# Optimization experiments

Measured on AMD Instinct MI355X. Metric: run time of the kernel, lower is better.

The kernel has to match this reference:

```python
import jax, jax.numpy as jnp
import numpy as np

D_MODEL = 1024
D_STATE = 128
D_CONV = 4
EXPAND = 2
HEADDIM = 64
D_INNER = EXPAND * D_MODEL          # 2048
NHEADS = D_INNER // HEADDIM          # 32
CONV_CH = D_INNER + 2 * D_STATE      # conv acts on x, B, C (ngroups=1)
D_IN_PROJ = 2 * D_INNER + 2 * D_STATE + NHEADS
CHUNK = 128


def setup_inputs() -> dict:
    key = jax.random.key(0)
    ks = jax.random.split(key, 8)
    B, L = 4, 2048
    return {
        'x': jax.random.normal(ks[0], (B, L, D_MODEL), jnp.float32),
        'ln_w': jnp.ones((D_MODEL,), jnp.float32),
        'ln_b': jnp.zeros((D_MODEL,), jnp.float32),
        'in_proj_w': jax.random.normal(ks[1], (D_IN_PROJ, D_MODEL), jnp.float32) * 0.02,
        'conv_w': jax.random.normal(ks[2], (CONV_CH, D_CONV), jnp.float32) * 0.2,
        'conv_b': jnp.zeros((CONV_CH,), jnp.float32),
        'dt_bias': jax.random.normal(ks[3], (NHEADS,), jnp.float32) * 0.5,
        'A_log': jax.random.uniform(ks[4], (NHEADS,), jnp.float32, 0.0, 1.5),
        'D': jax.random.normal(ks[5], (NHEADS,), jnp.float32) * 0.1 + 1.0,
        'norm_w': jnp.ones((D_INNER,), jnp.float32),
        'out_proj_w': jax.random.normal(ks[6], (D_MODEL, D_INNER), jnp.float32) * 0.02,
    }


def segsum(a):
    # a: (..., T) -> (..., T, T) with out[i, j] = sum_{j < k <= i} a[k], -inf above diag
    T = a.shape[-1]
    a_rep = jnp.broadcast_to(a[..., :, None], a.shape + (T,))
    a_masked = jnp.where(jnp.tril(jnp.ones((T, T), bool), -1), a_rep, 0.0)
    seg = jnp.cumsum(a_masked, axis=-2)
    return jnp.where(jnp.tril(jnp.ones((T, T), bool), 0), seg, -jnp.inf)


def _ssd(X, a, Bm, Cm):
    # Chunked SSD (Mamba2). X: (b,l,h,p) pre-multiplied by dt; a: (b,l,h)=dt*A; Bm,Cm: (b,l,n)
    b, l, h, p = X.shape
    c = l // CHUNK
    Xc = X.reshape(b, c, CHUNK, h, p)
    Bc = Bm.reshape(b, c, CHUNK, -1)
    Cc = Cm.reshape(b, c, CHUNK, -1)
    ac = a.reshape(b, c, CHUNK, h).transpose(0, 3, 1, 2)   # (b,h,c,q)
    a_cs = jnp.cumsum(ac, axis=-1)                          # (b,h,c,q)
    Lm = jnp.exp(segsum(ac))                                # (b,h,c,q,q)
    # intra-chunk (diagonal) part
    Y_diag = jnp.einsum('bcln,bcsn,bhcls,bcshp->bclhp', Cc, Bc, Lm, Xc)
    # chunk final states
    decay_states = jnp.exp(a_cs[..., -1:] - a_cs)           # (b,h,c,q)
    states = jnp.einsum('bcln,bhcl,bclhp->bchpn', Bc, decay_states, Xc)
    states = jnp.concatenate([jnp.zeros_like(states[:, :1]), states], axis=1)  # (b,c+1,h,p,n)
    a_chunk = jnp.pad(a_cs[..., -1], ((0, 0), (0, 0), (1, 0)))  # (b,h,c+1)
    decay_chunk = jnp.exp(segsum(a_chunk))                  # (b,h,c+1,c+1)
    prev_states = jnp.einsum('bhzc,bchpn->bzhpn', decay_chunk, states)[:, :-1]  # (b,c,h,p,n)
    # inter-chunk (off-diagonal) part
    Y_off = jnp.einsum('bcln,bchpn,bhcl->bclhp', Cc, prev_states, jnp.exp(a_cs))
    return (Y_diag + Y_off).reshape(b, l, h, p)


def reference(x, ln_w, ln_b, in_proj_w, conv_w, conv_b, dt_bias, A_log, D, norm_w, out_proj_w):
    B, L, _ = x.shape
    # pre-LayerNorm
    mu = x.mean(-1, keepdims=True)
    var = ((x - mu) ** 2).mean(-1, keepdims=True)
    h = (x - mu) / jnp.sqrt(var + 1e-5) * ln_w + ln_b
    # Mamba2 in_proj -> [z, xBC, dt]
    zxbcdt = h @ in_proj_w.T
    z = zxbcdt[..., :D_INNER]
    xBC = zxbcdt[..., D_INNER:D_INNER + CONV_CH]
    dt = jax.nn.softplus(zxbcdt[..., -NHEADS:] + dt_bias)  # (B,L,H)
    # causal depthwise conv1d + SiLU
    xp = jnp.pad(xBC, ((0, 0), (D_CONV - 1, 0), (0, 0)))
    conv = sum(xp[:, k:k + L, :] * conv_w[:, k] for k in range(D_CONV)) + conv_b
    xBC = jax.nn.silu(conv)
    xs = xBC[..., :D_INNER].reshape(B, L, NHEADS, HEADDIM)
    Bm = xBC[..., D_INNER:D_INNER + D_STATE]
    Cm = xBC[..., D_INNER + D_STATE:]
    A = -jnp.exp(A_log)                                    # (H,)
    Y = _ssd(xs * dt[..., None], dt * A, Bm, Cm)
    Y = Y + D[None, None, :, None] * xs                    # D skip connection
    y = Y.reshape(B, L, D_INNER)
    # gated RMSNorm (norm_before_gate=False)
    y = y * jax.nn.silu(z)
    y = y * jax.lax.rsqrt(jnp.mean(y * y, -1, keepdims=True) + 1e-5) * norm_w
    out = y @ out_proj_w.T
    # dropout in eval mode = identity; residual
    return out + x
```

## Files before the change

kernel.cpp:

```cpp
#include <hip/hip_runtime.h>
#include <math.h>

#define BATCH   4
#define LSEQ    2048
#define DMODEL  1024
#define DSTATE  128
#define HEADDIM 64
#define DINNER  2048
#define NHEADS  32
#define CONVCH  2304
#define DINPROJ 4384
#define NPAD    4480
#define CHUNKL  128
#define NCHUNK  16
#define ROWS    (BATCH*LSEQ)

#define B_Z     ((size_t)0)
#define B_XBC   (B_Z   + (size_t)ROWS*DINNER*2)
#define B_DT    (B_XBC + (size_t)ROWS*CONVCH*2)
#define B_XS    (B_DT  + (size_t)ROWS*NHEADS*4)
#define B_BC    (B_XS  + (size_t)ROWS*DINNER*2)
#define B_Y     (B_BC  + (size_t)ROWS*256*2)
#define B_ASUM  (B_Y   + (size_t)ROWS*DINNER*2)
#define B_END   (B_ASUM + (size_t)BATCH*NCHUNK*NHEADS*4)

typedef __attribute__((ext_vector_type(8))) short bf16x8;
typedef __attribute__((ext_vector_type(4))) float f32x4;

__device__ __forceinline__ float b2f(ushort u) {
  union { uint32_t i; float f; } v; v.i = ((uint32_t)u) << 16; return v.f;
}
__device__ __forceinline__ ushort f2b(float f) {
  union { float f; uint32_t i; } v; v.f = f;
  uint32_t r = (v.i + 0x7FFFu + ((v.i >> 16) & 1u)) >> 16;
  return (ushort)r;
}

__device__ __forceinline__ void async_ld16(const void* g, void* l) {
  __builtin_amdgcn_global_load_lds(
      (const __attribute__((address_space(1))) unsigned int*)g,
      (__attribute__((address_space(3))) unsigned int*)l, 16, 0, 0);
}

template<int K>
__device__ __forceinline__ void gemm_core_swz(const ushort* __restrict__ A,
    const ushort* __restrict__ W, int m0, int n0, int tid,
    ushort* lA, ushort* lB, f32x4 acc[4][4])
{
  const int lane = tid & 63;
  const int w = tid >> 6;
  const int wm = (w & 1) * 64;
  const int wn = (w >> 1) * 64;
  const int rl = lane & 15;
  const int q  = lane >> 4;
  for (int k0 = 0; k0 < K; k0 += 64) {
    __syncthreads();
    #pragma unroll
    for (int is = 0; is < 4; is++) {
      int s = (w*4 + is)*64 + lane;
      int row = s >> 3;
      int g = (s & 7) ^ (row & 7);
      async_ld16(A + (size_t)(m0 + row)*K + k0 + g*8, lA + (size_t)s*8);
      async_ld16(W + (size_t)(n0 + row)*K + k0 + g*8, lB + (size_t)s*8);
    }
    __syncthreads();
    #pragma unroll
    for (int kh = 0; kh < 2; kh++) {
      bf16x8 af[4], bfr[4];
      #pragma unroll
      for (int i = 0; i < 4; i++) {
        int row = wm + i*16 + rl;
        af[i] = *(const bf16x8*)&lA[(size_t)(row*8 + ((kh*4 + q) ^ (row & 7)))*8];
      }
      #pragma unroll
      for (int j = 0; j < 4; j++) {
        int row = wn + j*16 + rl;
        bfr[j] = *(const bf16x8*)&lB[(size_t)(row*8 + ((kh*4 + q) ^ (row & 7)))*8];
      }
      #pragma unroll
      for (int i = 0; i < 4; i++)
        #pragma unroll
        for (int j = 0; j < 4; j++)
          acc[i][j] = __builtin_amdgcn_mfma_f32_16x16x32_bf16(af[i], bfr[j], acc[i][j], 0, 0, 0);
    }
  }
}

__global__ __launch_bounds__(256) void convert_win_kernel(const float* __restrict__ W,
                                                          ushort* __restrict__ Wb)
{
  size_t i = (size_t)blockIdx.x*256 + threadIdx.x;
  Wb[i] = (i < (size_t)DINPROJ*DMODEL) ? f2b(W[i]) : (ushort)0;
}

__global__ __launch_bounds__(256) void convert_wout_kernel(const float* __restrict__ W,
                                                           ushort* __restrict__ Wb)
{
  size_t i = (size_t)blockIdx.x*256 + threadIdx.x;
  Wb[i] = f2b(W[i]);
}

__global__ __launch_bounds__(256) void ln_kernel(const float* __restrict__ x,
    const float* __restrict__ w, const float* __restrict__ bias, ushort* __restrict__ h)
{
  const int row = blockIdx.x;
  const int t = threadIdx.x;
  const float* xr = x + (size_t)row * DMODEL;
  float v[4];
  float s = 0.f;
  #pragma unroll
  for (int i = 0; i < 4; i++) { v[i] = xr[t + i*256]; s += v[i]; }
  __shared__ float red[4];
  #pragma unroll
  for (int o = 32; o > 0; o >>= 1) s += __shfl_down(s, o, 64);
  if ((t & 63) == 0) red[t >> 6] = s;
  __syncthreads();
  float mean = (red[0]+red[1]+red[2]+red[3]) * (1.f/DMODEL);
  float vs = 0.f;
  #pragma unroll
  for (int i = 0; i < 4; i++) { float d = v[i]-mean; vs += d*d; }
  #pragma unroll
  for (int o = 32; o > 0; o >>= 1) vs += __shfl_down(vs, o, 64);
  __syncthreads();
  if ((t & 63) == 0) red[t >> 6] = vs;
  __syncthreads();
  float rstd = rsqrtf((red[0]+red[1]+red[2]+red[3]) * (1.f/DMODEL) + 1e-5f);
  ushort* hr = h + (size_t)row * DMODEL;
  #pragma unroll
  for (int i = 0; i < 4; i++) {
    int c = t + i*256;
    hr[c] = f2b((v[i]-mean)*rstd*w[c] + bias[c]);
  }
}

__global__ __launch_bounds__(256) void gemm_inproj_mfma(const ushort* __restrict__ A,
    const ushort* __restrict__ W, ushort* __restrict__ z, ushort* __restrict__ xbc,
    float* __restrict__ dtr, const float* __restrict__ dtb)
{
  __shared__ ushort smem[16384];
  ushort* lA = smem;
  ushort* lB = smem + 8192;
  const int tid = threadIdx.x;
  const int lane = tid & 63;
  const int w = tid >> 6;
  const int m0 = blockIdx.x * 128;
  const int n0 = blockIdx.y * 128;
  const int wm = (w & 1) * 64;
  const int wn = (w >> 1) * 64;
  f32x4 acc[4][4];
  #pragma unroll
  for (int i = 0; i < 4; i++)
    #pragma unroll
    for (int j = 0; j < 4; j++) acc[i][j] = (f32x4)(0.f);

  gemm_core_swz<DMODEL>(A, W, m0, n0, tid, lA, lB, acc);

  const int col_l = lane & 15;
  const int row_l = (lane >> 4) * 4;
  __syncthreads();
  if (n0 < DINNER + CONVCH) {
    #pragma unroll
    for (int i = 0; i < 4; i++)
      #pragma unroll
      for (int j = 0; j < 4; j++) {
        int col = wn + j*16 + col_l;
        int g = col >> 3;
        #pragma unroll
        for (int r = 0; r < 4; r++) {
          int row = wm + i*16 + row_l + r;
          smem[row*128 + ((g ^ (row & 7)) << 3) + (col & 7)] = f2b(acc[i][j][r]);
        }
      }
    __syncthreads();
    ushort* outp; int coff, ncols;
    if (n0 < DINNER) { outp = z;   coff = n0;          ncols = DINNER; }
    else             { outp = xbc; coff = n0 - DINNER; ncols = CONVCH; }
    #pragma unroll
    for (int it = 0; it < 8; it++) {
      int idx = tid + it*256;
      int row = idx >> 4, c8 = idx & 15;
      *(uint4*)(outp + (size_t)(m0 + row)*ncols + coff + c8*8) =
          *(const uint4*)&smem[row*128 + ((c8 ^ (row & 7)) << 3)];
    }
  } else {
    #pragma unroll
    for (int i = 0; i < 4; i++)
      #pragma unroll
      for (int j = 0; j < 2; j++) {
        int lc = wn + j*16 + col_l;
        if (lc < 32) {
          float bb = dtb[lc];
          #pragma unroll
          for (int r = 0; r < 4; r++) {
            float v = acc[i][j][r] + bb;
            v = (v > 20.f) ? v : log1pf(expf(v));
            dtr[(size_t)(m0 + wm + i*16 + row_l + r)*NHEADS + lc] = v;
          }
        }
      }
  }
}

__global__ __launch_bounds__(256) void gemm_outproj_mfma(const ushort* __restrict__ A,
    const ushort* __restrict__ W, const float* __restrict__ x, float* __restrict__ out)
{
  __shared__ ushort smem[16384];
  ushort* lA = smem;
  ushort* lB = smem + 8192;
  float* fbuf = (float*)smem;
  const int tid = threadIdx.x;
  const int lane = tid & 63;
  const int w = tid >> 6;
  const int m0 = blockIdx.x * 128;
  const int n0 = blockIdx.y * 128;
  const int wn = (w >> 1) * 64;
  f32x4 acc[4][4];
  #pragma unroll
  for (int i = 0; i < 4; i++)
    #pragma unroll
    for (int j = 0; j < 4; j++) acc[i][j] = (f32x4)(0.f);

  gemm_core_swz<DINNER>(A, W, m0, n0, tid, lA, lB, acc);

  const int colL = lane & 15;
  const int rowQ = (lane >> 4) * 4;
  #pragma unroll
  for (int h0 = 0; h0 < 2; h0++) {
    __syncthreads();
    if ((w & 1) == h0) {
      #pragma unroll
      for (int i = 0; i < 4; i++)
        #pragma unroll
        for (int j = 0; j < 4; j++) {
          int col = wn + j*16 + colL;
          int g = col >> 2;
          #pragma unroll
          for (int r = 0; r < 4; r++) {
            int row = i*16 + rowQ + r;
            fbuf[row*128 + ((g ^ (row & 7)) << 2) + (col & 3)] = acc[i][j][r];
          }
        }
    }
    __syncthreads();
    #pragma unroll
    for (int it = 0; it < 8; it++) {
      int idx = tid + it*256;
      int row = idx >> 5, c4 = idx & 31;
      int gm = m0 + h0*64 + row;
      float4 xv = *(const float4*)(x + (size_t)gm*DMODEL + n0 + c4*4);
      float4 vv = *(const float4*)&fbuf[row*128 + ((c4 ^ (row & 7)) << 2)];
      vv.x += xv.x; vv.y += xv.y; vv.z += xv.z; vv.w += xv.w;
      *(float4*)(out + (size_t)gm*DMODEL + n0 + c4*4) = vv;
    }
  }
}

__global__ __launch_bounds__(256) void conv_tiled(const ushort* __restrict__ xbc,
    const float* __restrict__ cw, const float* __restrict__ cb,
    ushort* __restrict__ xs, ushort* __restrict__ bcb)
{
  __shared__ ushort tile[35*256];
  const int tid = threadIdx.x;
  const int ch0 = blockIdx.x * 256;
  const int row0 = blockIdx.y * 32;
  const int l0 = row0 & (LSEQ-1);
  for (int idx = tid; idx < 35*32; idx += 256) {
    int r = idx >> 5, c16 = idx & 31;
    uint4 v = make_uint4(0,0,0,0);
    if (l0 + r - 3 >= 0)
      v = *(const uint4*)(xbc + (size_t)(row0 + r - 3)*CONVCH + ch0 + c16*8);
    *(uint4*)&tile[r*256 + c16*8] = v;
  }
  __syncthreads();
  const int ch = ch0 + tid;
  const float w0 = cw[ch*4+0], w1 = cw[ch*4+1], w2 = cw[ch*4+2], w3 = cw[ch*4+3];
  const float bias = cb[ch];
  const bool isX = (ch0 < DINNER);
  #pragma unroll 4
  for (int r = 0; r < 32; r++) {
    float acc = bias;
    acc = fmaf(b2f(tile[(r+0)*256 + tid]), w0, acc);
    acc = fmaf(b2f(tile[(r+1)*256 + tid]), w1, acc);
    acc = fmaf(b2f(tile[(r+2)*256 + tid]), w2, acc);
    acc = fmaf(b2f(tile[(r+3)*256 + tid]), w3, acc);
    float v = acc / (1.f + expf(-acc));
    if (isX) xs[(size_t)(row0 + r)*DINNER + ch] = f2b(v);
    else     bcb[(size_t)(row0 + r)*256 + (ch - DINNER)] = f2b(v);
  }
}

__global__ __launch_bounds__(256) void states_mfma(
    const ushort* __restrict__ xs, const ushort* __restrict__ bcb, const float* __restrict__ dt,
    const float* __restrict__ A_log, ushort* __restrict__ S, float* __restrict__ asum)
{
  constexpr int LDP = 136;
  __shared__ ushort lBT[128*LDP];
  __shared__ ushort lXT[64*LDP];
  __shared__ float dts[CHUNKL], acs[CHUNKL];
  __shared__ float wtot;
  const int hh = blockIdx.x, c = blockIdx.y, b = blockIdx.z;
  const int tid = threadIdx.x;
  const int lane = tid & 63;
  const int w = tid >> 6;
  const int rbase = b*LSEQ + c*CHUNKL;
  const size_t sbase = (size_t)((b*NCHUNK + c)*NHEADS + hh) * 8192;

  float pre = 0.f;
  if (tid < 128) {
    float myv = dt[(size_t)(rbase + tid)*NHEADS + hh];
    dts[tid] = myv;
    pre = myv;
    #pragma unroll
    for (int o = 1; o < 64; o <<= 1) {
      float u = __shfl_up(pre, o, 64);
      if ((tid & 63) >= o) pre += u;
    }
    if (tid == 63) wtot = pre;
  }
  #pragma unroll
  for (int it = 0; it < 8; it++) {
    int chunk = tid + it*256;
    int l = chunk >> 4, n8 = chunk & 15;
    ushort tmp[8];
    *(uint4*)tmp = *(const uint4*)(bcb + (size_t)(rbase + l)*256 + n8*8);
    #pragma unroll
    for (int u = 0; u < 8; u++) lBT[(n8*8+u)*LDP + l] = tmp[u];
  }
  __syncthreads();
  float alast_loc = 0.f;
  if (tid < 128) {
    float Aval = -expf(A_log[hh]);
    float a = (pre + ((tid >= 64) ? wtot : 0.f)) * Aval;
    acs[tid] = a;
    if (tid == 127) { asum[(b*NCHUNK + c)*NHEADS + hh] = a; }
  }
  __syncthreads();
  alast_loc = acs[CHUNKL-1];
  #pragma unroll
  for (int it = 0; it < 4; it++) {
    int chunk = tid + it*256;
    int l = chunk >> 3, p8 = (chunk & 7)*8;
    ushort tmp[8];
    *(uint4*)tmp = *(const uint4*)(xs + (size_t)(rbase + l)*DINNER + hh*HEADDIM + p8);
    float wl = dts[l] * expf(alast_loc - acs[l]);
    #pragma unroll
    for (int u = 0; u < 8; u++) lXT[(p8+u)*LDP + l] = f2b(b2f(tmp[u]) * wl);
  }
  __syncthreads();

  const int rl = lane & 15;
  const int kq = (lane >> 4) * 8;
  const int nb = w * 32;
  f32x4 acc[4][2];
  #pragma unroll
  for (int i = 0; i < 4; i++) { acc[i][0] = (f32x4)(0.f); acc[i][1] = (f32x4)(0.f); }
  #pragma unroll
  for (int k0 = 0; k0 < 128; k0 += 32) {
    bf16x8 af[4], bfr[2];
    #pragma unroll
    for (int i = 0; i < 4; i++) af[i]  = *(const bf16x8*)&lXT[(i*16 + rl)*LDP + k0 + kq];
    #pragma unroll
    for (int j = 0; j < 2; j++) bfr[j] = *(const bf16x8*)&lBT[(nb + j*16 + rl)*LDP + k0 + kq];
    #pragma unroll
    for (int i = 0; i < 4; i++)
      #pragma unroll
      for (int j = 0; j < 2; j++)
        acc[i][j] = __builtin_amdgcn_mfma_f32_16x16x32_bf16(af[i], bfr[j], acc[i][j], 0, 0, 0);
  }
  __syncthreads();
  const int colL = lane & 15;
  const int rowQ = (lane >> 4) * 4;
  #pragma unroll
  for (int i = 0; i < 4; i++)
    #pragma unroll
    for (int j = 0; j < 2; j++)
      #pragma unroll
      for (int r = 0; r < 4; r++)
        lXT[(i*16 + rowQ + r)*LDP + nb + j*16 + colL] = f2b(acc[i][j][r]);
  __syncthreads();
  #pragma unroll
  for (int it = 0; it < 4; it++) {
    int idx = tid + it*256;
    int row = idx >> 4, c8 = idx & 15;
    *(uint4*)(S + sbase + row*128 + c8*8) = *(const uint4*)&lXT[row*LDP + c8*8];
  }
}

__global__ __launch_bounds__(256) void scan_kernel(ushort* __restrict__ S, const float* __restrict__ asum)
{
  const int hh = blockIdx.x, sl = blockIdx.y, b = blockIdx.z;
  const int base0 = sl*2048 + threadIdx.x;
  float carry[8];
  #pragma unroll
  for (int i = 0; i < 8; i++) carry[i] = 0.f;
  for (int c = 0; c < NCHUNK; c++) {
    ushort* Sp = S + (size_t)((b*NCHUNK + c)*NHEADS + hh) * 8192;
    float dec = expf(asum[(b*NCHUNK + c)*NHEADS + hh]);
    #pragma unroll
    for (int i = 0; i < 8; i++) {
      int idx = base0 + i*256;
      float sv = b2f(Sp[idx]);
      Sp[idx] = f2b(carry[i]);
      carry[i] = fmaf(dec, carry[i], sv);
    }
  }
}

__global__ __launch_bounds__(256) void yssd_mfma(
    const ushort* __restrict__ xs, const ushort* __restrict__ bcb, const float* __restrict__ dt,
    const float* __restrict__ A_log, const float* __restrict__ Dvec,
    const ushort* __restrict__ S, ushort* __restrict__ y)
{
  constexpr int LDP = 136;
  __shared__ ushort lM [128*LDP];
  __shared__ ushort lXT[64*LDP];
  __shared__ float dts[CHUNKL], acs[CHUNKL];
  __shared__ float wtot;
  const int hh = blockIdx.x, c = blockIdx.y, b = blockIdx.z;
  const int tid = threadIdx.x;
  const int lane = tid & 63;
  const int w = tid >> 6;
  const int rbase = b*LSEQ + c*CHUNKL;
  const size_t sbase = (size_t)((b*NCHUNK + c)*NHEADS + hh) * 8192;
  const ushort* Bg = bcb + (size_t)rbase*256;
  const ushort* Cg = Bg + 128;

  #pragma unroll
  for (int it = 0; it < 4; it++) {
    int chunk = tid + it*256;
    int s = chunk >> 3, p0 = (chunk & 7)*8;
    ushort tmp[8];
    *(uint4*)tmp = *(const uint4*)(xs + (size_t)(rbase + s)*DINNER + hh*HEADDIM + p0);
    #pragma unroll
    for (int u = 0; u < 8; u++) lXT[(p0+u)*LDP + s] = tmp[u];
  }
  float pre = 0.f;
  if (tid < 128) {
    float myv = dt[(size_t)(rbase + tid)*NHEADS + hh];
    dts[tid] = myv;
    pre = myv;
    #pragma unroll
    for (int o = 1; o < 64; o <<= 1) {
      float u = __shfl_up(pre, o, 64);
      if ((tid & 63) >= o) pre += u;
    }
    if (tid == 63) wtot = pre;
  }
  __syncthreads();
  if (tid < 128) {
    float Aval = -expf(A_log[hh]);
    acs[tid] = (pre + ((tid >= 64) ? wtot : 0.f)) * Aval;
  }

  const int rl = lane & 15;
  const int kq = (lane >> 4) * 8;
  const int colL = lane & 15;
  const int rowQ = (lane >> 4) * 4;

  const int wm = (w & 1) * 64;
  const int wn = (w >> 1) * 64;
  f32x4 G[4][4];
  #pragma unroll
  for (int i = 0; i < 4; i++)
    #pragma unroll
    for (int j = 0; j < 4; j++) G[i][j] = (f32x4)(0.f);
  #pragma unroll
  for (int k0 = 0; k0 < 128; k0 += 32) {
    bf16x8 af[4], bfr[4];
    #pragma unroll
    for (int i = 0; i < 4; i++) af[i]  = *(const bf16x8*)(Cg + (size_t)(wm + i*16 + rl)*256 + k0 + kq);
    #pragma unroll
    for (int j = 0; j < 4; j++) bfr[j] = *(const bf16x8*)(Bg + (size_t)(wn + j*16 + rl)*256 + k0 + kq);
    #pragma unroll
    for (int i = 0; i < 4; i++)
      #pragma unroll
      for (int j = 0; j < 4; j++)
        G[i][j] = __builtin_amdgcn_mfma_f32_16x16x32_bf16(af[i], bfr[j], G[i][j], 0, 0, 0);
  }
  __syncthreads();

  #pragma unroll
  for (int j = 0; j < 4; j++) {
    int sIdx = wn + j*16 + colL;
    float as = acs[sIdx];
    float ds = dts[sIdx];
    #pragma unroll
    for (int i = 0; i < 4; i++) {
      #pragma unroll
      for (int r = 0; r < 4; r++) {
        int lIdx = wm + i*16 + rowQ + r;
        float m = (lIdx >= sIdx) ? G[i][j][r] * expf(acs[lIdx] - as) * ds : 0.f;
        lM[lIdx*LDP + sIdx] = f2b(m);
      }
    }
  }

  const int om = w * 32;
  f32x4 Y[2][4];
  #pragma unroll
  for (int i = 0; i < 2; i++)
    #pragma unroll
    for (int j = 0; j < 4; j++) Y[i][j] = (f32x4)(0.f);
  #pragma unroll
  for (int k0 = 0; k0 < 128; k0 += 32) {
    bf16x8 a2[2], b2[4];
    #pragma unroll
    for (int i = 0; i < 2; i++) a2[i] = *(const bf16x8*)(Cg + (size_t)(om + i*16 + rl)*256 + k0 + kq);
    #pragma unroll
    for (int j = 0; j < 4; j++) b2[j] = *(const bf16x8*)(S + sbase + (size_t)(j*16 + rl)*128 + k0 + kq);
    #pragma unroll
    for (int i = 0; i < 2; i++)
      #pragma unroll
      for (int j = 0; j < 4; j++)
        Y[i][j] = __builtin_amdgcn_mfma_f32_16x16x32_bf16(a2[i], b2[j], Y[i][j], 0, 0, 0);
  }
  #pragma unroll
  for (int i = 0; i < 2; i++)
    #pragma unroll
    for (int r = 0; r < 4; r++) {
      float e = expf(acs[om + i*16 + rowQ + r]);
      #pragma unroll
      for (int j = 0; j < 4; j++) Y[i][j][r] *= e;
    }
  __syncthreads();

  #pragma unroll
  for (int k0 = 0; k0 < 128; k0 += 32) {
    bf16x8 a3[2], b3[4];
    #pragma unroll
    for (int i = 0; i < 2; i++) a3[i] = *(const bf16x8*)&lM[(om + i*16 + rl)*LDP + k0 + kq];
    #pragma unroll
    for (int j = 0; j < 4; j++) b3[j] = *(const bf16x8*)&lXT[(j*16 + rl)*LDP + k0 + kq];
    #pragma unroll
    for (int i = 0; i < 2; i++)
      #pragma unroll
      for (int j = 0; j < 4; j++)
        Y[i][j] = __builtin_amdgcn_mfma_f32_16x16x32_bf16(a3[i], b3[j], Y[i][j], 0, 0, 0);
  }

  const float Dh = Dvec[hh];
  #pragma unroll
  for (int i = 0; i < 2; i++) {
    #pragma unroll
    for (int r = 0; r < 4; r++) {
      int lIdx = om + i*16 + rowQ + r;
      ushort* yrow = y + (size_t)(rbase + lIdx)*DINNER + hh*HEADDIM;
      #pragma unroll
      for (int j = 0; j < 4; j++) {
        int p = j*16 + colL;
        float val = Y[i][j][r] + Dh * b2f(lXT[p*LDP + lIdx]);
        yrow[p] = f2b(val);
      }
    }
  }
}

__global__ __launch_bounds__(256) void rmsnorm_kernel(ushort* __restrict__ y,
    const ushort* __restrict__ z, const float* __restrict__ nw)
{
  const int row = blockIdx.x;
  const int t = threadIdx.x;
  ushort* yr = y + (size_t)row*DINNER;
  const ushort* zr = z + (size_t)row*DINNER;
  float v[8];
  float ss = 0.f;
  #pragma unroll
  for (int i = 0; i < 8; i++) {
    int c = t + i*256;
    float zz = b2f(zr[c]);
    float g = b2f(yr[c]) * (zz / (1.f + expf(-zz)));
    v[i] = g;
    ss += g*g;
  }
  #pragma unroll
  for (int o = 32; o > 0; o >>= 1) ss += __shfl_down(ss, o, 64);
  __shared__ float red[4];
  if ((t & 63) == 0) red[t >> 6] = ss;
  __syncthreads();
  float scale = rsqrtf((red[0]+red[1]+red[2]+red[3]) * (1.f/DINNER) + 1e-5f);
  #pragma unroll
  for (int i = 0; i < 8; i++) {
    int c = t + i*256;
    yr[c] = f2b(v[i]*scale*nw[c]);
  }
}

extern "C" void kernel_launch(void* const* d_in, const int* in_sizes, int n_in,
                              void* d_out, int out_size, void* d_ws, size_t ws_size,
                              hipStream_t stream)
{
  const float* x    = (const float*)d_in[0];
  const float* lnw  = (const float*)d_in[1];
  const float* lnb  = (const float*)d_in[2];
  const float* win  = (const float*)d_in[3];
  const float* cw   = (const float*)d_in[4];
  const float* cb   = (const float*)d_in[5];
  const float* dtb  = (const float*)d_in[6];
  const float* alog = (const float*)d_in[7];
  const float* dvec = (const float*)d_in[8];
  const float* nw   = (const float*)d_in[9];
  const float* wout = (const float*)d_in[10];
  float* out = (float*)d_out;
  char* ws = (char*)d_ws;
  (void)in_sizes; (void)n_in; (void)out_size;

  if (ws_size < B_END) return;

  ushort* zb   = (ushort*)(ws + B_Z);
  ushort* xbcb = (ushort*)(ws + B_XBC);
  float*  dtr  = (float*) (ws + B_DT);
  ushort* xsb  = (ushort*)(ws + B_XS);
  ushort* bcb  = (ushort*)(ws + B_BC);
  ushort* yb   = (ushort*)(ws + B_Y);
  float*  asum = (float*) (ws + B_ASUM);
  ushort* Sb   = xbcb;
  ushort* hb   = yb;
  ushort* winB = (ushort*)(ws + B_Y + (size_t)ROWS*DMODEL*2);
  ushort* woutB= (ushort*)(ws + B_XBC + (size_t)BATCH*NCHUNK*NHEADS*HEADDIM*DSTATE*2);

  hipLaunchKernelGGL(convert_win_kernel, dim3((NPAD*DMODEL)/256), dim3(256), 0, stream, win, winB);
  hipLaunchKernelGGL(ln_kernel, dim3(ROWS), dim3(256), 0, stream, x, lnw, lnb, hb);
  hipLaunchKernelGGL(gemm_inproj_mfma, dim3(64, 35), dim3(256), 0, stream, hb, winB, zb, xbcb, dtr, dtb);
  hipLaunchKernelGGL(conv_tiled, dim3(9, ROWS/32), dim3(256), 0, stream, xbcb, cw, cb, xsb, bcb);
  hipLaunchKernelGGL(convert_wout_kernel, dim3((DMODEL*DINNER)/256), dim3(256), 0, stream, wout, woutB);
  hipLaunchKernelGGL(states_mfma, dim3(NHEADS, NCHUNK, BATCH), dim3(256), 0, stream,
                     xsb, bcb, dtr, alog, Sb, asum);
  hipLaunchKernelGGL(scan_kernel, dim3(NHEADS, 4, BATCH), dim3(256), 0, stream, Sb, asum);
  hipLaunchKernelGGL(yssd_mfma, dim3(NHEADS, NCHUNK, BATCH), dim3(256), 0, stream,
                     xsb, bcb, dtr, alog, dvec, Sb, yb);
  hipLaunchKernelGGL(rmsnorm_kernel, dim3(ROWS), dim3(256), 0, stream, yb, zb, nw);
  hipLaunchKernelGGL(gemm_outproj_mfma, dim3(64, 8), dim3(256), 0, stream, yb, woutB, x, out);
}
```

Baseline: 459.6 us.

## Register-prefetch GEMM tiles and scan states instead of direct-to-LDS loads

Result: slower. 793.6 us (+72.7%).

```diff
diff --git a/kernel.cpp b/kernel.cpp
--- a/kernel.cpp
+++ b/kernel.cpp
@@ -36,14 +36,8 @@
   return (ushort)r;
 }
 
-__device__ __forceinline__ void async_ld16(const void* g, void* l) {
-  __builtin_amdgcn_global_load_lds(
-      (const __attribute__((address_space(1))) unsigned int*)g,
-      (__attribute__((address_space(3))) unsigned int*)l, 16, 0, 0);
-}
-
 template<int K>
-__device__ __forceinline__ void gemm_core_swz(const ushort* __restrict__ A,
+__device__ __forceinline__ void gemm_core_pipe(const ushort* __restrict__ A,
     const ushort* __restrict__ W, int m0, int n0, int tid,
     ushort* lA, ushort* lB, f32x4 acc[4][4])
 {
@@ -53,17 +47,34 @@
   const int wn = (w >> 1) * 64;
   const int rl = lane & 15;
   const int q  = lane >> 4;
+  int srow[4], sgr[4];
+  #pragma unroll
+  for (int is = 0; is < 4; is++) {
+    int s = w*256 + is*64 + lane;
+    srow[is] = s >> 3;
+    sgr[is]  = (s & 7) ^ ((s >> 3) & 7);
+  }
+  uint4 ra[4], rb[4];
+  #pragma unroll
+  for (int is = 0; is < 4; is++) {
+    ra[is] = *(const uint4*)(A + (size_t)(m0 + srow[is])*K + sgr[is]*8);
+    rb[is] = *(const uint4*)(W + (size_t)(n0 + srow[is])*K + sgr[is]*8);
+  }
   for (int k0 = 0; k0 < K; k0 += 64) {
+    #pragma unroll
+    for (int is = 0; is < 4; is++) {
+      int s = w*256 + is*64 + lane;
+      *(uint4*)&lA[(size_t)s*8] = ra[is];
+      *(uint4*)&lB[(size_t)s*8] = rb[is];
+    }
     __syncthreads();
-    #pragma unroll
-    for (int is = 0; is < 4; is++) {
-      int s = (w*4 + is)*64 + lane;
-      int row = s >> 3;
-      int g = (s & 7) ^ (row & 7);
-      async_ld16(A + (size_t)(m0 + row)*K + k0 + g*8, lA + (size_t)s*8);
-      async_ld16(W + (size_t)(n0 + row)*K + k0 + g*8, lB + (size_t)s*8);
-    }
-    __syncthreads();
+    if (k0 + 64 < K) {
+      #pragma unroll
+      for (int is = 0; is < 4; is++) {
+        ra[is] = *(const uint4*)(A + (size_t)(m0 + srow[is])*K + (k0 + 64) + sgr[is]*8);
+        rb[is] = *(const uint4*)(W + (size_t)(n0 + srow[is])*K + (k0 + 64) + sgr[is]*8);
+      }
+    }
     #pragma unroll
     for (int kh = 0; kh < 2; kh++) {
       bf16x8 af[4], bfr[4];
@@ -83,6 +94,7 @@
         for (int j = 0; j < 4; j++)
           acc[i][j] = __builtin_amdgcn_mfma_f32_16x16x32_bf16(af[i], bfr[j], acc[i][j], 0, 0, 0);
     }
+    __syncthreads();
   }
 }
 
@@ -153,7 +165,7 @@
     #pragma unroll
     for (int j = 0; j < 4; j++) acc[i][j] = (f32x4)(0.f);
 
-  gemm_core_swz<DMODEL>(A, W, m0, n0, tid, lA, lB, acc);
+  gemm_core_pipe<DMODEL>(A, W, m0, n0, tid, lA, lB, acc);
 
   const int col_l = lane & 15;
   const int row_l = (lane >> 4) * 4;
@@ -220,7 +232,7 @@
     #pragma unroll
     for (int j = 0; j < 4; j++) acc[i][j] = (f32x4)(0.f);
 
-  gemm_core_swz<DINNER>(A, W, m0, n0, tid, lA, lB, acc);
+  gemm_core_pipe<DINNER>(A, W, m0, n0, tid, lA, lB, acc);
 
   const int colL = lane & 15;
   const int rowQ = (lane >> 4) * 4;
@@ -390,18 +402,32 @@
 {
   const int hh = blockIdx.x, sl = blockIdx.y, b = blockIdx.z;
   const int base0 = sl*2048 + threadIdx.x;
+  float decs[NCHUNK];
+  #pragma unroll
+  for (int c = 0; c < NCHUNK; c++) decs[c] = asum[(b*NCHUNK + c)*NHEADS + hh];
+  #pragma unroll
+  for (int c = 0; c < NCHUNK; c++) decs[c] = expf(decs[c]);
   float carry[8];
   #pragma unroll
   for (int i = 0; i < 8; i++) carry[i] = 0.f;
+  ushort cur[8], nxt[8];
+  ushort* Sp0 = S + (size_t)((b*NCHUNK + 0)*NHEADS + hh) * 8192;
+  #pragma unroll
+  for (int i = 0; i < 8; i++) cur[i] = Sp0[base0 + i*256];
   for (int c = 0; c < NCHUNK; c++) {
     ushort* Sp = S + (size_t)((b*NCHUNK + c)*NHEADS + hh) * 8192;
-    float dec = expf(asum[(b*NCHUNK + c)*NHEADS + hh]);
+    if (c + 1 < NCHUNK) {
+      ushort* Sn = S + (size_t)((b*NCHUNK + c + 1)*NHEADS + hh) * 8192;
+      #pragma unroll
+      for (int i = 0; i < 8; i++) nxt[i] = Sn[base0 + i*256];
+    }
+    float dec = decs[c];
     #pragma unroll
     for (int i = 0; i < 8; i++) {
-      int idx = base0 + i*256;
-      float sv = b2f(Sp[idx]);
-      Sp[idx] = f2b(carry[i]);
+      float sv = b2f(cur[i]);
+      Sp[base0 + i*256] = f2b(carry[i]);
       carry[i] = fmaf(dec, carry[i], sv);
+      cur[i] = nxt[i];
     }
   }
 }
```
